# Optimization experiments

Measured on AMD Instinct MI355X. Metric: run time of the kernel, lower is better.

Reference implementation:

```python
import jax, jax.numpy as jnp
import numpy as np

N_NODES = 100000
N_EDGES = 1600000
IN_C, HID_C, OUT_C = 128, 128, 64


def setup_inputs() -> dict:
    key = jax.random.key(0)
    ks = jax.random.split(key, 8)
    x = jax.random.normal(ks[0], (N_NODES, IN_C), dtype=jnp.float32)
    edge_index = jax.random.randint(ks[1], (2, N_EDGES), 0, N_NODES, dtype=jnp.int64)
    # SAGEConv params: lin_l (aggregated neighbors, with bias), lin_r (root, no bias)
    s1 = 1.0 / np.sqrt(IN_C)
    s2 = 1.0 / np.sqrt(HID_C)
    W1_l = jax.random.uniform(ks[2], (IN_C, HID_C), jnp.float32, -s1, s1)
    b1_l = jnp.zeros((HID_C,), jnp.float32)
    W1_r = jax.random.uniform(ks[3], (IN_C, HID_C), jnp.float32, -s1, s1)
    W2_l = jax.random.uniform(ks[4], (HID_C, OUT_C), jnp.float32, -s2, s2)
    b2_l = jnp.zeros((OUT_C,), jnp.float32)
    W2_r = jax.random.uniform(ks[5], (HID_C, OUT_C), jnp.float32, -s2, s2)
    return {"x": x, "edge_index": edge_index, "W1_l": W1_l, "b1_l": b1_l,
            "W1_r": W1_r, "W2_l": W2_l, "b2_l": b2_l, "W2_r": W2_r}


def _sage_conv(x, src, dst, W_l, b_l, W_r):
    # gather source features, scatter-max reduce onto destinations
    msg = x[src]                                             # [E, C]
    aggr = jax.ops.segment_max(msg, dst, num_segments=N_NODES)
    aggr = jnp.where(jnp.isfinite(aggr), aggr, 0.0)          # isolated nodes -> 0 (PyG behavior)
    return aggr @ W_l + b_l + x @ W_r


def reference(x, edge_index, W1_l, b1_l, W1_r, W2_l, b2_l, W2_r):
    src, dst = edge_index[0], edge_index[1]
    h = _sage_conv(x, src, dst, W1_l, b1_l, W1_r)
    h = jax.nn.relu(h)
    # dropout is identity in eval mode
    out = _sage_conv(h, src, dst, W2_l, b2_l, W2_r)
    return out
```

## Files before the change

### kernel.cpp

```cpp
#include <hip/hip_runtime.h>
#include <cstdint>
#include <cmath>

#define NNODES 100000
#define NEDGES 1600000
#define NBKT   196
#define CAP    9216
#define BIN_CHUNK 4096

typedef __attribute__((ext_vector_type(8))) __bf16 bf16x8;
typedef __attribute__((ext_vector_type(4))) float f32x4;

__device__ __forceinline__ unsigned short f2bf_rne(float f) {
    unsigned int u = __float_as_uint(f);
    u += 0x7fffu + ((u >> 16) & 1u);
    return (unsigned short)(u >> 16);
}

__global__ __launch_bounds__(256) void zero_kernel(int* __restrict__ p, int n) {
    int i = blockIdx.x * 256 + threadIdx.x;
    if (i < n) p[i] = 0;
}

__global__ __launch_bounds__(256) void convert_bf16_kernel(const float4* __restrict__ in,
                                                           uint2* __restrict__ out, int n4) {
    int i = blockIdx.x * 256 + threadIdx.x;
    if (i >= n4) return;
    float4 v = in[i];
    uint2 o;
    o.x = (unsigned)f2bf_rne(v.x) | ((unsigned)f2bf_rne(v.y) << 16);
    o.y = (unsigned)f2bf_rne(v.z) | ((unsigned)f2bf_rne(v.w) << 16);
    out[i] = o;
}

__global__ __launch_bounds__(256) void bin_kernel(
        const int* __restrict__ src, const int* __restrict__ dst,
        unsigned int* __restrict__ binArr, int* __restrict__ bucketFill, int nE) {
    __shared__ unsigned int stage[BIN_CHUNK];
    __shared__ unsigned char bof[BIN_CHUNK];
    __shared__ int cnt[256], cstart[256], cfill[256], gbase[256];
    const int tid = threadIdx.x;
    const int blockStart = blockIdx.x * BIN_CHUNK;
    const int chunkN = min(BIN_CHUNK, nE - blockStart);

    cnt[tid] = 0;
    __syncthreads();

    int myd[16], mys[16];
#pragma unroll
    for (int i = 0; i < 16; ++i) {
        int idx = i * 256 + tid;
        if (idx < chunkN) {
            myd[i] = dst[blockStart + idx];
            mys[i] = src[blockStart + idx];
            atomicAdd(&cnt[myd[i] >> 9], 1);
        }
    }
    __syncthreads();
    int v = cnt[tid];
    for (int off = 1; off < 256; off <<= 1) {
        int add = (tid >= off) ? cnt[tid - off] : 0;
        __syncthreads();
        cnt[tid] += add;
        __syncthreads();
    }
    cstart[tid] = cnt[tid] - v;
    cfill[tid] = cnt[tid] - v;
    if (tid < NBKT && v > 0) gbase[tid] = atomicAdd(&bucketFill[tid], v);
    __syncthreads();
#pragma unroll
    for (int i = 0; i < 16; ++i) {
        int idx = i * 256 + tid;
        if (idx < chunkN) {
            int b = myd[i] >> 9;
            int p = atomicAdd(&cfill[b], 1);
            stage[p] = ((unsigned)(myd[i] & 511) << 17) | (unsigned)mys[i];
            bof[p] = (unsigned char)b;
        }
    }
    __syncthreads();
#pragma unroll
    for (int i = 0; i < 16; ++i) {
        int idx = i * 256 + tid;
        if (idx < chunkN) {
            int b = bof[idx];
            int slot = gbase[b] + (idx - cstart[b]);
            if (slot < CAP) binArr[(size_t)b * CAP + slot] = stage[idx];
        }
    }
}

__global__ __launch_bounds__(512) void build_csr_kernel(
        const unsigned int* __restrict__ binArr, const int* __restrict__ bucketFill,
        unsigned int* __restrict__ sortedSrc,
        int* __restrict__ rowBeg, int* __restrict__ rowEnd) {
    __shared__ unsigned int stage[CAP];
    __shared__ int ncnt[512], nstart[512];
    const int b = blockIdx.x;
    const int t = threadIdx.x;
    const int cnt_b = min(bucketFill[b], CAP);

    ncnt[t] = 0;
    __syncthreads();
    for (int i = t; i < cnt_b; i += 512) {
        unsigned int e = binArr[(size_t)b * CAP + i];
        stage[i] = e;
        atomicAdd(&ncnt[e >> 17], 1);
    }
    __syncthreads();
    int v = ncnt[t];
    for (int off = 1; off < 512; off <<= 1) {
        int add = (t >= off) ? ncnt[t - off] : 0;
        __syncthreads();
        ncnt[t] += add;
        __syncthreads();
    }
    int start = ncnt[t] - v;
    nstart[t] = start;
    int n = (b << 9) + t;
    if (n < NNODES) {
        rowBeg[n] = b * CAP + start;
        rowEnd[n] = b * CAP + start + v;
    }
    __syncthreads();
    for (int i = t; i < cnt_b; i += 512) {
        unsigned int e = stage[i];
        int p = atomicAdd(&nstart[e >> 17], 1);
        sortedSrc[(size_t)b * CAP + p] = e & 0x1FFFFu;
    }
}

__global__ __launch_bounds__(256) void aggregate_max_bf16_v2(
        const uint4* __restrict__ xb,
        const int* __restrict__ rowBeg,
        const int* __restrict__ rowEnd,
        const unsigned int* __restrict__ sortedSrc,
        uint4* __restrict__ aggrb, int nN) {
    const int wave = threadIdx.x >> 6;
    const int lane = threadIdx.x & 63;
    const int n = blockIdx.x * 4 + wave;
    if (n >= nN) return;
    const int beg = rowBeg[n];
    const int end = rowEnd[n];
    const int grp = lane >> 4;
    const int c16 = lane & 15;

    if (end == beg) {
        if (lane < 16) {
            uint4 z; z.x = z.y = z.z = z.w = 0u;
            aggrb[(size_t)n * 16 + lane] = z;
        }
        return;
    }

    float acc[8];
#pragma unroll
    for (int i = 0; i < 8; ++i) acc[i] = -INFINITY;

    const int last = end - 1;
    for (int base = beg; base < end; base += 64) {
        int idx = base + lane;
        int myid = (int)sortedSrc[idx <= last ? idx : last];
        int m = end - base; if (m > 64) m = 64;
        for (int j = 0; j < m; j += 8) {
            int s0 = __shfl(myid, j + grp);
            int s1 = __shfl(myid, j + 4 + grp);
            uint4 p0 = xb[(size_t)s0 * 16 + c16];
            uint4 p1 = xb[(size_t)s1 * 16 + c16];
            unsigned int u[8] = {p0.x, p0.y, p0.z, p0.w, p1.x, p1.y, p1.z, p1.w};
#pragma unroll
            for (int q = 0; q < 8; ++q) {
                float fe = __uint_as_float(u[q] << 16);
                float fo = __uint_as_float(u[q] & 0xffff0000u);
                int c = (q & 3) * 2;
                acc[c]     = fmaxf(acc[c],     fe);
                acc[c + 1] = fmaxf(acc[c + 1], fo);
            }
        }
    }
#pragma unroll
    for (int i = 0; i < 8; ++i) {
        float v = acc[i];
        v = fmaxf(v, __shfl_xor(v, 16));
        v = fmaxf(v, __shfl_xor(v, 32));
        acc[i] = v;
    }
    if (lane < 16) {
        uint4 o;
        o.x = (__float_as_uint(acc[1]) & 0xffff0000u) | (__float_as_uint(acc[0]) >> 16);
        o.y = (__float_as_uint(acc[3]) & 0xffff0000u) | (__float_as_uint(acc[2]) >> 16);
        o.z = (__float_as_uint(acc[5]) & 0xffff0000u) | (__float_as_uint(acc[4]) >> 16);
        o.w = (__float_as_uint(acc[7]) & 0xffff0000u) | (__float_as_uint(acc[6]) >> 16);
        aggrb[(size_t)n * 16 + c16] = o;
    }
}

template<int BN, bool RELU, typename OutT>
__global__ __launch_bounds__(256) void sage_gemm_mfma(
        const unsigned short* __restrict__ Aagg,
        const unsigned short* __restrict__ Aroot,
        const float* __restrict__ Wl,
        const float* __restrict__ Wr,
        const float* __restrict__ bias,
        OutT* __restrict__ C,
        int M) {
    constexpr int KP = 136;
    constexpr int NT = BN / 16;
    __shared__ __align__(16) unsigned short Bs[BN * KP];

    const int tid = threadIdx.x;
    const int wave = tid >> 6;
    const int lane = tid & 63;
    const int quad = lane >> 4;
    const int mrow = lane & 15;

    const int rowA = blockIdx.x * 64 + wave * 16 + mrow;
    const int rowAc = (rowA < M) ? rowA : 0;
    const int rowD = blockIdx.x * 64 + wave * 16 + quad * 4;

    f32x4 acc[NT];
#pragma unroll
    for (int nt = 0; nt < NT; ++nt) acc[nt] = (f32x4){0.f, 0.f, 0.f, 0.f};

    for (int half = 0; half < 2; ++half) {
        const float* W = half ? Wr : Wl;
        const unsigned short* Asrc = half ? Aroot : Aagg;
        __syncthreads();
        for (int i = tid; i < BN * 128; i += 256) {
            int n = i % BN;
            int k = i / BN;
            Bs[n * KP + k] = f2bf_rne(W[k * BN + n]);
        }
        __syncthreads();
#pragma unroll
        for (int kt = 0; kt < 4; ++kt) {
            bf16x8 a = *(const bf16x8*)(Asrc + (size_t)rowAc * 128 + kt * 32 + quad * 8);
#pragma unroll
            for (int nt = 0; nt < NT; ++nt) {
                bf16x8 b = *(const bf16x8*)(&Bs[(nt * 16 + mrow) * KP + kt * 32 + quad * 8]);
                acc[nt] = __builtin_amdgcn_mfma_f32_16x16x32_bf16(a, b, acc[nt], 0, 0, 0);
            }
        }
    }

#pragma unroll
    for (int nt = 0; nt < NT; ++nt) {
        int col = nt * 16 + mrow;
        float bv = bias[col];
#pragma unroll
        for (int r = 0; r < 4; ++r) {
            int grow = rowD + r;
            if (grow < M) {
                float v = acc[nt][r] + bv;
                if (RELU) v = fmaxf(v, 0.0f);
                if constexpr (sizeof(OutT) == 2)
                    C[(size_t)grow * BN + col] = (OutT)f2bf_rne(v);
                else
                    C[(size_t)grow * BN + col] = (OutT)v;
            }
        }
    }
}

extern "C" void kernel_launch(void* const* d_in, const int* in_sizes, int n_in,
                              void* d_out, int out_size, void* d_ws, size_t ws_size,
                              hipStream_t stream) {
    const float* x   = (const float*)d_in[0];
    const int*   ei  = (const int*)d_in[1];
    const float* W1l = (const float*)d_in[2];
    const float* b1l = (const float*)d_in[3];
    const float* W1r = (const float*)d_in[4];
    const float* W2l = (const float*)d_in[5];
    const float* b2l = (const float*)d_in[6];
    const float* W2r = (const float*)d_in[7];
    float* out = (float*)d_out;

    const int* src = ei;
    const int* dst = ei + NEDGES;

    char* ws = (char*)d_ws;
    unsigned short* xb    = (unsigned short*)ws; ws += (size_t)NNODES * 128 * 2;
    unsigned short* hb    = (unsigned short*)ws; ws += (size_t)NNODES * 128 * 2;
    unsigned short* aggrb = (unsigned short*)ws; ws += (size_t)NNODES * 128 * 2;
    unsigned int* binArr    = (unsigned int*)ws; ws += (size_t)NBKT * CAP * 4;
    unsigned int* sortedSrc = (unsigned int*)ws; ws += (size_t)NBKT * CAP * 4;
    int* rowBeg     = (int*)ws; ws += (size_t)NNODES * 4;
    int* rowEnd     = (int*)ws; ws += (size_t)NNODES * 4;
    int* bucketFill = (int*)ws; ws += 256 * 4;

    const int gAgg = (NNODES + 3) / 4;
    const int gGemm = (NNODES + 63) / 64;
    const int n4 = NNODES * 128 / 4;
    const int gBin = (NEDGES + BIN_CHUNK - 1) / BIN_CHUNK;

    zero_kernel<<<1, 256, 0, stream>>>(bucketFill, 256);
    convert_bf16_kernel<<<(n4 + 255) / 256, 256, 0, stream>>>((const float4*)x, (uint2*)xb, n4);
    bin_kernel<<<gBin, 256, 0, stream>>>(src, dst, binArr, bucketFill, NEDGES);
    build_csr_kernel<<<NBKT, 512, 0, stream>>>(binArr, bucketFill, sortedSrc, rowBeg, rowEnd);

    aggregate_max_bf16_v2<<<gAgg, 256, 0, stream>>>((const uint4*)xb, rowBeg, rowEnd, sortedSrc,
                                                    (uint4*)aggrb, NNODES);
    sage_gemm_mfma<128, true, unsigned short><<<gGemm, 256, 0, stream>>>(
        aggrb, xb, W1l, W1r, b1l, hb, NNODES);
    aggregate_max_bf16_v2<<<gAgg, 256, 0, stream>>>((const uint4*)hb, rowBeg, rowEnd, sortedSrc,
                                                    (uint4*)aggrb, NNODES);
    sage_gemm_mfma<64, false, float><<<gGemm, 256, 0, stream>>>(
        aggrb, hb, W2l, W2r, b2l, out, NNODES);
}
```

Before: 311.6 us.

## Encode bf16 as order-preserving int16 for packed max; pre-transpose weights once

Features are stored in a sign-magnitude-flipped bf16 encoding so that max over bf16 values becomes a packed signed 16-bit integer max. Each gathered uint4 then needs four packed max ops instead of unpacking to floats. The GEMM decodes the root operand on load, and layer 1 writes its output already encoded. A separate small kernel converts and transposes the weights to bf16 once, so each GEMM block copies them into shared memory instead of converting them per block. The cost is encode/decode ALU work in the GEMM and the conversion kernels. NaN handling may also differ slightly from the float max path.

```diff
diff --git a/kernel.cpp b/kernel.cpp
--- a/kernel.cpp
+++ b/kernel.cpp
@@ -7,9 +7,11 @@
 #define NBKT   196
 #define CAP    9216
 #define BIN_CHUNK 4096
+#define KP 136
 
 typedef __attribute__((ext_vector_type(8))) __bf16 bf16x8;
 typedef __attribute__((ext_vector_type(4))) float f32x4;
+typedef short v2s __attribute__((ext_vector_type(2)));
 
 __device__ __forceinline__ unsigned short f2bf_rne(float f) {
     unsigned int u = __float_as_uint(f);
@@ -17,20 +19,47 @@
     return (unsigned short)(u >> 16);
 }
 
+__device__ __forceinline__ unsigned encdec(unsigned u) {
+    return u ^ (((u & 0x80008000u) >> 15) * 0x7FFFu);
+}
+
+__device__ __forceinline__ unsigned pkmax(unsigned a, unsigned b) {
+    v2s r = __builtin_elementwise_max(__builtin_bit_cast(v2s, a), __builtin_bit_cast(v2s, b));
+    return __builtin_bit_cast(unsigned, r);
+}
+
 __global__ __launch_bounds__(256) void zero_kernel(int* __restrict__ p, int n) {
     int i = blockIdx.x * 256 + threadIdx.x;
     if (i < n) p[i] = 0;
 }
 
-__global__ __launch_bounds__(256) void convert_bf16_kernel(const float4* __restrict__ in,
-                                                           uint2* __restrict__ out, int n4) {
+__global__ __launch_bounds__(256) void convert_encode_kernel(const float4* __restrict__ in,
+                                                             uint2* __restrict__ out, int n4) {
     int i = blockIdx.x * 256 + threadIdx.x;
     if (i >= n4) return;
     float4 v = in[i];
     uint2 o;
-    o.x = (unsigned)f2bf_rne(v.x) | ((unsigned)f2bf_rne(v.y) << 16);
-    o.y = (unsigned)f2bf_rne(v.z) | ((unsigned)f2bf_rne(v.w) << 16);
+    o.x = encdec((unsigned)f2bf_rne(v.x) | ((unsigned)f2bf_rne(v.y) << 16));
+    o.y = encdec((unsigned)f2bf_rne(v.z) | ((unsigned)f2bf_rne(v.w) << 16));
     out[i] = o;
+}
+
+__global__ __launch_bounds__(256) void convert_weights_kernel(
+        const float* __restrict__ W1l, const float* __restrict__ W1r,
+        const float* __restrict__ W2l, const float* __restrict__ W2r,
+        unsigned short* __restrict__ T1l, unsigned short* __restrict__ T1r,
+        unsigned short* __restrict__ T2l, unsigned short* __restrict__ T2r) {
+    int i = blockIdx.x * 256 + threadIdx.x;
+    if (i < 128 * 128) {
+        int k = i >> 7, n = i & 127;
+        T1l[n * KP + k] = f2bf_rne(W1l[i]);
+        T1r[n * KP + k] = f2bf_rne(W1r[i]);
+    }
+    if (i < 128 * 64) {
+        int k = i >> 6, n = i & 63;
+        T2l[n * KP + k] = f2bf_rne(W2l[i]);
+        T2r[n * KP + k] = f2bf_rne(W2r[i]);
+    }
 }
 
 __global__ __launch_bounds__(256) void bin_kernel(
@@ -130,8 +159,8 @@
     }
 }
 
-__global__ __launch_bounds__(256) void aggregate_max_bf16_v2(
-        const uint4* __restrict__ xb,
+__global__ __launch_bounds__(256) void aggregate_max_pk(
+        const uint4* __restrict__ xe,
         const int* __restrict__ rowBeg,
         const int* __restrict__ rowEnd,
         const unsigned int* __restrict__ sortedSrc,
@@ -153,9 +182,9 @@
         return;
     }
 
-    float acc[8];
-#pragma unroll
-    for (int i = 0; i < 8; ++i) acc[i] = -INFINITY;
+    unsigned accp[4];
+#pragma unroll
+    for (int i = 0; i < 4; ++i) accp[i] = 0x80008000u;
 
     const int last = end - 1;
     for (int base = beg; base < end; base += 64) {
@@ -165,46 +194,44 @@
         for (int j = 0; j < m; j += 8) {
             int s0 = __shfl(myid, j + grp);
             int s1 = __shfl(myid, j + 4 + grp);
-            uint4 p0 = xb[(size_t)s0 * 16 + c16];
-            uint4 p1 = xb[(size_t)s1 * 16 + c16];
-            unsigned int u[8] = {p0.x, p0.y, p0.z, p0.w, p1.x, p1.y, p1.z, p1.w};
-#pragma unroll
-            for (int q = 0; q < 8; ++q) {
-                float fe = __uint_as_float(u[q] << 16);
-                float fo = __uint_as_float(u[q] & 0xffff0000u);
-                int c = (q & 3) * 2;
-                acc[c]     = fmaxf(acc[c],     fe);
-                acc[c + 1] = fmaxf(acc[c + 1], fo);
-            }
-        }
-    }
-#pragma unroll
-    for (int i = 0; i < 8; ++i) {
-        float v = acc[i];
-        v = fmaxf(v, __shfl_xor(v, 16));
-        v = fmaxf(v, __shfl_xor(v, 32));
-        acc[i] = v;
+            uint4 p0 = xe[(size_t)s0 * 16 + c16];
+            uint4 p1 = xe[(size_t)s1 * 16 + c16];
+            accp[0] = pkmax(accp[0], p0.x);
+            accp[1] = pkmax(accp[1], p0.y);
+            accp[2] = pkmax(accp[2], p0.z);
+            accp[3] = pkmax(accp[3], p0.w);
+            accp[0] = pkmax(accp[0], p1.x);
+            accp[1] = pkmax(accp[1], p1.y);
+            accp[2] = pkmax(accp[2], p1.z);
+            accp[3] = pkmax(accp[3], p1.w);
+        }
+    }
+#pragma unroll
+    for (int i = 0; i < 4; ++i) {
+        unsigned v = accp[i];
+        v = pkmax(v, (unsigned)__shfl_xor((int)v, 16));
+        v = pkmax(v, (unsigned)__shfl_xor((int)v, 32));
+        accp[i] = v;
     }
     if (lane < 16) {
         uint4 o;
-        o.x = (__float_as_uint(acc[1]) & 0xffff0000u) | (__float_as_uint(acc[0]) >> 16);
-        o.y = (__float_as_uint(acc[3]) & 0xffff0000u) | (__float_as_uint(acc[2]) >> 16);
-        o.z = (__float_as_uint(acc[5]) & 0xffff0000u) | (__float_as_uint(acc[4]) >> 16);
-        o.w = (__float_as_uint(acc[7]) & 0xffff0000u) | (__float_as_uint(acc[6]) >> 16);
+        o.x = encdec(accp[0]);
+        o.y = encdec(accp[1]);
+        o.z = encdec(accp[2]);
+        o.w = encdec(accp[3]);
         aggrb[(size_t)n * 16 + c16] = o;
     }
 }
 
-template<int BN, bool RELU, typename OutT>
+template<int BN, bool RELU, bool ENCOUT, typename OutT>
 __global__ __launch_bounds__(256) void sage_gemm_mfma(
         const unsigned short* __restrict__ Aagg,
         const unsigned short* __restrict__ Aroot,
-        const float* __restrict__ Wl,
-        const float* __restrict__ Wr,
+        const unsigned short* __restrict__ Wtl,
+        const unsigned short* __restrict__ Wtr,
         const float* __restrict__ bias,
         OutT* __restrict__ C,
         int M) {
-    constexpr int KP = 136;
     constexpr int NT = BN / 16;
     __shared__ __align__(16) unsigned short Bs[BN * KP];
 
@@ -223,18 +250,20 @@
     for (int nt = 0; nt < NT; ++nt) acc[nt] = (f32x4){0.f, 0.f, 0.f, 0.f};
 
     for (int half = 0; half < 2; ++half) {
-        const float* W = half ? Wr : Wl;
-        const unsigned short* Asrc = half ? Aroot : Aagg;
-        __syncthreads();
-        for (int i = tid; i < BN * 128; i += 256) {
-            int n = i % BN;
-            int k = i / BN;
-            Bs[n * KP + k] = f2bf_rne(W[k * BN + n]);
-        }
+        const uint4* wsrc = (const uint4*)(half ? Wtr : Wtl);
+        __syncthreads();
+        for (int i = tid; i < BN * KP / 8; i += 256) ((uint4*)Bs)[i] = wsrc[i];
         __syncthreads();
 #pragma unroll
         for (int kt = 0; kt < 4; ++kt) {
-            bf16x8 a = *(const bf16x8*)(Asrc + (size_t)rowAc * 128 + kt * 32 + quad * 8);
+            bf16x8 a;
+            if (half == 0) {
+                a = *(const bf16x8*)(Aagg + (size_t)rowAc * 128 + kt * 32 + quad * 8);
+            } else {
+                uint4 t = *(const uint4*)(Aroot + (size_t)rowAc * 128 + kt * 32 + quad * 8);
+                t.x = encdec(t.x); t.y = encdec(t.y); t.z = encdec(t.z); t.w = encdec(t.w);
+                a = __builtin_bit_cast(bf16x8, t);
+            }
 #pragma unroll
             for (int nt = 0; nt < NT; ++nt) {
                 bf16x8 b = *(const bf16x8*)(&Bs[(nt * 16 + mrow) * KP + kt * 32 + quad * 8]);
@@ -253,10 +282,13 @@
             if (grow < M) {
                 float v = acc[nt][r] + bv;
                 if (RELU) v = fmaxf(v, 0.0f);
-                if constexpr (sizeof(OutT) == 2)
-                    C[(size_t)grow * BN + col] = (OutT)f2bf_rne(v);
-                else
+                if constexpr (ENCOUT) {
+                    unsigned u = f2bf_rne(v);
+                    u ^= ((u >> 15) & 1u) * 0x7FFFu;
+                    C[(size_t)grow * BN + col] = (OutT)u;
+                } else {
                     C[(size_t)grow * BN + col] = (OutT)v;
+                }
             }
         }
     }
@@ -279,14 +311,18 @@
     const int* dst = ei + NEDGES;
 
     char* ws = (char*)d_ws;
-    unsigned short* xb    = (unsigned short*)ws; ws += (size_t)NNODES * 128 * 2;
-    unsigned short* hb    = (unsigned short*)ws; ws += (size_t)NNODES * 128 * 2;
+    unsigned short* xe    = (unsigned short*)ws; ws += (size_t)NNODES * 128 * 2;
+    unsigned short* he    = (unsigned short*)ws; ws += (size_t)NNODES * 128 * 2;
     unsigned short* aggrb = (unsigned short*)ws; ws += (size_t)NNODES * 128 * 2;
     unsigned int* binArr    = (unsigned int*)ws; ws += (size_t)NBKT * CAP * 4;
     unsigned int* sortedSrc = (unsigned int*)ws; ws += (size_t)NBKT * CAP * 4;
     int* rowBeg     = (int*)ws; ws += (size_t)NNODES * 4;
     int* rowEnd     = (int*)ws; ws += (size_t)NNODES * 4;
     int* bucketFill = (int*)ws; ws += 256 * 4;
+    unsigned short* T1l = (unsigned short*)ws; ws += 128 * KP * 2;
+    unsigned short* T1r = (unsigned short*)ws; ws += 128 * KP * 2;
+    unsigned short* T2l = (unsigned short*)ws; ws += 64 * KP * 2;
+    unsigned short* T2r = (unsigned short*)ws; ws += 64 * KP * 2;
 
     const int gAgg = (NNODES + 3) / 4;
     const int gGemm = (NNODES + 63) / 64;
@@ -294,16 +330,17 @@
     const int gBin = (NEDGES + BIN_CHUNK - 1) / BIN_CHUNK;
 
     zero_kernel<<<1, 256, 0, stream>>>(bucketFill, 256);
-    convert_bf16_kernel<<<(n4 + 255) / 256, 256, 0, stream>>>((const float4*)x, (uint2*)xb, n4);
+    convert_weights_kernel<<<64, 256, 0, stream>>>(W1l, W1r, W2l, W2r, T1l, T1r, T2l, T2r);
+    convert_encode_kernel<<<(n4 + 255) / 256, 256, 0, stream>>>((const float4*)x, (uint2*)xe, n4);
     bin_kernel<<<gBin, 256, 0, stream>>>(src, dst, binArr, bucketFill, NEDGES);
     build_csr_kernel<<<NBKT, 512, 0, stream>>>(binArr, bucketFill, sortedSrc, rowBeg, rowEnd);
 
-    aggregate_max_bf16_v2<<<gAgg, 256, 0, stream>>>((const uint4*)xb, rowBeg, rowEnd, sortedSrc,
-                                                    (uint4*)aggrb, NNODES);
-    sage_gemm_mfma<128, true, unsigned short><<<gGemm, 256, 0, stream>>>(
-        aggrb, xb, W1l, W1r, b1l, hb, NNODES);
-    aggregate_max_bf16_v2<<<gAgg, 256, 0, stream>>>((const uint4*)hb, rowBeg, rowEnd, sortedSrc,
-                                                    (uint4*)aggrb, NNODES);
-    sage_gemm_mfma<64, false, float><<<gGemm, 256, 0, stream>>>(
-        aggrb, hb, W2l, W2r, b2l, out, NNODES);
-}
+    aggregate_max_pk<<<gAgg, 256, 0, stream>>>((const uint4*)xe, rowBeg, rowEnd, sortedSrc,
+                                               (uint4*)aggrb, NNODES);
+    sage_gemm_mfma<128, true, true, unsigned short><<<gGemm, 256, 0, stream>>>(
+        aggrb, xe, T1l, T1r, b1l, he, NNODES);
+    aggregate_max_pk<<<gAgg, 256, 0, stream>>>((const uint4*)he, rowBeg, rowEnd, sortedSrc,
+                                               (uint4*)aggrb, NNODES);
+    sage_gemm_mfma<64, false, false, float><<<gGemm, 256, 0, stream>>>(
+        aggrb, he, T2l, T2r, b2l, out, NNODES);
+}
```

Result: no change. 306.5 us (-1.6%).
